# Kernel optimization log

Hardware: AMD Instinct MI355X
Metric: run time of the kernel (lower is better)

Reference implementation:

```python
import jax, jax.numpy as jnp
import numpy as np

B, S, N, H, E = 512, 96, 64, 512, 512  # batch, seq_len, nodes(c_in), hidden, edges/graph


def setup_inputs() -> dict:
    key = jax.random.key(0)
    ks = jax.random.split(key, 6)
    x = jax.random.normal(ks[0], (B, S, N), jnp.float32)
    edge_index = jax.random.randint(ks[1], (B, 2, E), 0, N, dtype=jnp.int32)
    W1 = jax.random.normal(ks[2], (H, S), jnp.float32) * 0.05   # gcn1 lin weight [out,in]
    b1 = jnp.zeros((H,), jnp.float32)
    W2 = jax.random.normal(ks[3], (S, H), jnp.float32) * 0.05   # gcn2 lin weight
    b2 = jnp.zeros((S,), jnp.float32)
    conv_w = jax.random.normal(ks[4], (H, N, 3), jnp.float32) * 0.05  # Conv1d [out,in,k]
    return {"x": x, "edge_index": edge_index, "W1": W1, "b1": b1,
            "W2": W2, "b2": b2, "conv_w": conv_w}


def _gcn(h, src, dst, W, b, n):
    # PyG GCNConv: h' = D^-1/2 (A+I) D^-1/2 (h W^T) + b  (self-loops already in src/dst)
    h = h @ W.T                                       # [n, out]
    ones = jnp.ones(src.shape[0], h.dtype)
    deg = jax.ops.segment_sum(ones, dst, num_segments=n)
    dinv = jnp.where(deg > 0, jax.lax.rsqrt(deg), 0.0)
    norm = dinv[src] * dinv[dst]                      # [e]
    out = jax.ops.segment_sum(h[src] * norm[:, None], dst, num_segments=n)
    return out + b


def reference(x, edge_index, W1, b1, W2, b2, conv_w):
    b, s, n = x.shape
    loops = jnp.broadcast_to(jnp.arange(n, dtype=edge_index.dtype), (b, n))
    src = jnp.concatenate([edge_index[:, 0, :], loops], axis=1)  # add self-loops
    dst = jnp.concatenate([edge_index[:, 1, :], loops], axis=1)

    def per_graph(xb, sb, db):
        h = _gcn(xb.T, sb, db, W1, b1, n)   # [n, H]
        h = jax.nn.relu(h)
        h = _gcn(h, sb, db, W2, b2, n)      # [n, s]
        return h                             # channels-first [c_in, L]

    h = jax.vmap(per_graph)(x, src, dst)    # [b, n, s]
    # TokenEmbedding: Conv1d kernel=3, circular padding=1, no bias
    hp = jnp.pad(h, ((0, 0), (0, 0), (1, 1)), mode='wrap')
    y = jax.lax.conv_general_dilated(hp, conv_w, (1,), 'VALID',
                                     dimension_numbers=('NCH', 'OIH', 'NCH'))  # [b, H, s]
    return jnp.transpose(y, (0, 2, 1))      # [b, s, H]; dropout = identity (eval)
```

## Files before the change

### kernel.cpp

```cpp
#include <hip/hip_runtime.h>
#include <hip/hip_bf16.h>

#define BB 512
#define SS 96
#define NN 64
#define HH 512
#define EE 512

typedef __attribute__((ext_vector_type(8))) short short8;
typedef __attribute__((ext_vector_type(4))) float f32x4;

__device__ __forceinline__ unsigned short f2bf(float f) {
    union { float f; unsigned u; } v; v.f = f;
    return (unsigned short)((v.u + 0x7FFFu + ((v.u >> 16) & 1u)) >> 16);
}
__device__ __forceinline__ ushort4 f4bf(float4 v) {
    ushort4 u; u.x = f2bf(v.x); u.y = f2bf(v.y); u.z = f2bf(v.z); u.w = f2bf(v.w);
    return u;
}

__global__ __launch_bounds__(256) void k_mega(const float* __restrict__ x,
                                              const int* __restrict__ ei,
                                              const float* __restrict__ W1,
                                              const float* __restrict__ b1,
                                              const float* __restrict__ W2,
                                              const float* __restrict__ b2,
                                              unsigned short* __restrict__ H2T) {
    const int b = blockIdx.x, t = threadIdx.x;
    const int wave = t >> 6, lane = t & 63, quad = lane >> 4, l16 = lane & 15;

    __shared__ __align__(16) char smem[59392];
    unsigned short* As   = (unsigned short*)smem;
    unsigned short* XsW2 = (unsigned short*)(smem + 9216);
    unsigned short* Gs   = (unsigned short*)(smem + 23040);
    unsigned short* W1sT = (unsigned short*)(smem + 36352);
    float*          Asm  = (float*)(smem + 36352);
    unsigned short* H1s  = (unsigned short*)(smem + 49664);
    int*            deg  = (int*)(smem + 58880);
    float*          dinv = (float*)(smem + 59136);

    for (int i = t; i < 4096; i += 256) Asm[i] = 0.f;
    if (t < NN) deg[t] = 1;
    __syncthreads();
    const int* eb = ei + (size_t)b * 2 * EE;
    for (int e = t; e < EE; e += 256) atomicAdd(&deg[eb[EE + e]], 1);
    __syncthreads();
    if (t < NN) dinv[t] = rsqrtf((float)deg[t]);
    __syncthreads();
    for (int e = t; e < EE; e += 256) {
        int s = eb[e], d = eb[EE + e];
        atomicAdd(&Asm[d * 64 + s], dinv[s] * dinv[d]);
    }
    if (t < NN) atomicAdd(&Asm[t * 64 + t], dinv[t] * dinv[t]);
    __syncthreads();

    for (int i = t; i < 1024; i += 256) {
        int n = i >> 4, m4 = (i & 15) * 4;
        *(ushort4*)(As + n * 72 + m4) = f4bf(*(const float4*)(Asm + n * 64 + m4));
    }
    const float* xb = x + (size_t)b * SS * NN;
    for (int i = t; i < 96 * 16; i += 256) {
        int s = i >> 4, c4 = (i & 15) * 4;
        *(ushort4*)(XsW2 + s * 72 + c4) = f4bf(*(const float4*)(xb + s * 64 + c4));
    }
    __syncthreads();

    {
        short8 a0 = *(const short8*)(As + (wave * 16 + l16) * 72 + quad * 8);
        short8 a1 = *(const short8*)(As + (wave * 16 + l16) * 72 + 32 + quad * 8);
        f32x4 acc0[6];
        #pragma unroll
        for (int j = 0; j < 6; ++j) acc0[j] = (f32x4){0.f, 0.f, 0.f, 0.f};
        #pragma unroll
        for (int j = 0; j < 6; ++j) {
            short8 bb0 = *(const short8*)(XsW2 + (j * 16 + l16) * 72 + quad * 8);
            short8 bb1 = *(const short8*)(XsW2 + (j * 16 + l16) * 72 + 32 + quad * 8);
            acc0[j] = __builtin_amdgcn_mfma_f32_16x16x32_bf16(a0, bb0, acc0[j], 0, 0, 0);
            acc0[j] = __builtin_amdgcn_mfma_f32_16x16x32_bf16(a1, bb1, acc0[j], 0, 0, 0);
        }
        #pragma unroll
        for (int j = 0; j < 6; ++j)
            #pragma unroll
            for (int r = 0; r < 4; ++r)
                Gs[(wave * 16 + quad * 4 + r) * 104 + j * 16 + l16] = f2bf(acc0[j][r]);
    }

    f32x4 accT[6];
    #pragma unroll
    for (int j = 0; j < 6; ++j) accT[j] = (f32x4){0.f, 0.f, 0.f, 0.f};

    for (int hc = 0; hc < 8; ++hc) {
        __syncthreads();
        for (int i = t; i < 64 * 24; i += 256) {
            int row = i / 24, c4 = (i % 24) * 4;
            *(ushort4*)(W1sT + row * 104 + c4) =
                f4bf(*(const float4*)(W1 + (size_t)(hc * 64 + row) * 96 + c4));
        }
        for (int i = t; i < 96 * 16; i += 256) {
            int row = i >> 4, c4 = (i & 15) * 4;
            *(ushort4*)(XsW2 + row * 72 + c4) =
                f4bf(*(const float4*)(W2 + (size_t)row * HH + hc * 64 + c4));
        }
        __syncthreads();
        short8 ga[3];
        #pragma unroll
        for (int kc = 0; kc < 3; ++kc)
            ga[kc] = *(const short8*)(Gs + (wave * 16 + l16) * 104 + kc * 32 + quad * 8);
        f32x4 acc1[4];
        #pragma unroll
        for (int j = 0; j < 4; ++j) acc1[j] = (f32x4){0.f, 0.f, 0.f, 0.f};
        #pragma unroll
        for (int j = 0; j < 4; ++j)
            #pragma unroll
            for (int kc = 0; kc < 3; ++kc) {
                short8 bb = *(const short8*)(W1sT + (j * 16 + l16) * 104 + kc * 32 + quad * 8);
                acc1[j] = __builtin_amdgcn_mfma_f32_16x16x32_bf16(ga[kc], bb, acc1[j], 0, 0, 0);
            }
        float bias[4];
        #pragma unroll
        for (int j = 0; j < 4; ++j) bias[j] = b1[hc * 64 + j * 16 + l16];
        #pragma unroll
        for (int j = 0; j < 4; ++j)
            #pragma unroll
            for (int r = 0; r < 4; ++r)
                H1s[(wave * 16 + quad * 4 + r) * 72 + j * 16 + l16] =
                    f2bf(fmaxf(acc1[j][r] + bias[j], 0.f));
        __syncthreads();
        short8 ha0 = *(const short8*)(H1s + (wave * 16 + l16) * 72 + quad * 8);
        short8 ha1 = *(const short8*)(H1s + (wave * 16 + l16) * 72 + 32 + quad * 8);
        #pragma unroll
        for (int j = 0; j < 6; ++j) {
            short8 bb0 = *(const short8*)(XsW2 + (j * 16 + l16) * 72 + quad * 8);
            short8 bb1 = *(const short8*)(XsW2 + (j * 16 + l16) * 72 + 32 + quad * 8);
            accT[j] = __builtin_amdgcn_mfma_f32_16x16x32_bf16(ha0, bb0, accT[j], 0, 0, 0);
            accT[j] = __builtin_amdgcn_mfma_f32_16x16x32_bf16(ha1, bb1, accT[j], 0, 0, 0);
        }
    }
    __syncthreads();

    #pragma unroll
    for (int j = 0; j < 6; ++j)
        #pragma unroll
        for (int r = 0; r < 4; ++r)
            W1sT[(j * 16 + l16) * 72 + wave * 16 + quad * 4 + r] = f2bf(accT[j][r]);
    __syncthreads();

    {
        short8 a0 = *(const short8*)(As + (wave * 16 + l16) * 72 + quad * 8);
        short8 a1 = *(const short8*)(As + (wave * 16 + l16) * 72 + 32 + quad * 8);
        f32x4 acc3[6];
        #pragma unroll
        for (int j = 0; j < 6; ++j) acc3[j] = (f32x4){0.f, 0.f, 0.f, 0.f};
        #pragma unroll
        for (int j = 0; j < 6; ++j) {
            short8 t0 = *(const short8*)(W1sT + (j * 16 + l16) * 72 + quad * 8);
            short8 t1 = *(const short8*)(W1sT + (j * 16 + l16) * 72 + 32 + quad * 8);
            acc3[j] = __builtin_amdgcn_mfma_f32_16x16x32_bf16(a0, t0, acc3[j], 0, 0, 0);
            acc3[j] = __builtin_amdgcn_mfma_f32_16x16x32_bf16(a1, t1, acc3[j], 0, 0, 0);
        }
        unsigned short* Hb = H2T + (size_t)b * SS * NN;
        #pragma unroll
        for (int j = 0; j < 6; ++j) {
            float bb2 = b2[j * 16 + l16];
            #pragma unroll
            for (int r = 0; r < 4; ++r)
                Hb[(j * 16 + l16) * NN + wave * 16 + quad * 4 + r] = f2bf(acc3[j][r] + bb2);
        }
    }
}

__global__ __launch_bounds__(256) void k_conv(const unsigned short* __restrict__ H2T,
                                              const float* __restrict__ cw,
                                              float* __restrict__ out) {
    const int hb = blockIdx.x, b = blockIdx.y, t = threadIdx.x;
    const int wave = t >> 6, lane = t & 63, quad = lane >> 4, l16 = lane & 15;
    const int h0 = hb * 64;

    __shared__ __align__(16) unsigned short Wc[64 * 200];
    __shared__ __align__(16) unsigned short Hp[98 * 72];

    for (int i = t; i < 64 * 48; i += 256) {
        int row = i / 48, c4 = (i % 48) * 4;
        float4 v = *(const float4*)(cw + (size_t)(h0 + row) * 192 + c4);
        float vv[4] = {v.x, v.y, v.z, v.w};
        #pragma unroll
        for (int q = 0; q < 4; ++q) {
            int kap = c4 + q, n = kap / 3, kw = kap % 3;
            Wc[row * 200 + kw * 64 + n] = f2bf(vv[q]);
        }
    }
    const unsigned short* Hsrc = H2T + (size_t)b * SS * NN;
    for (int i = t; i < 98 * 8; i += 256) {
        int sp = i >> 3, c8 = (i & 7) * 8;
        int s = (sp == 0) ? 95 : ((sp == 97) ? 0 : sp - 1);
        *(short8*)(Hp + sp * 72 + c8) = *(const short8*)(Hsrc + s * NN + c8);
    }
    __syncthreads();

    short8 a[6];
    #pragma unroll
    for (int kc = 0; kc < 6; ++kc)
        a[kc] = *(const short8*)(Wc + (wave * 16 + l16) * 200 + kc * 32 + quad * 8);

    f32x4 acc[6];
    #pragma unroll
    for (int j = 0; j < 6; ++j) acc[j] = (f32x4){0.f, 0.f, 0.f, 0.f};

    #pragma unroll
    for (int j = 0; j < 6; ++j) {
        #pragma unroll
        for (int kc = 0; kc < 6; ++kc) {
            int kw = kc >> 1, nb = (kc & 1) * 32;
            int sp = j * 16 + l16 + kw;
            short8 bf = *(const short8*)(Hp + sp * 72 + nb + quad * 8);
            acc[j] = __builtin_amdgcn_mfma_f32_16x16x32_bf16(a[kc], bf, acc[j], 0, 0, 0);
        }
    }

    float* ob = out + (size_t)b * SS * HH;
    #pragma unroll
    for (int j = 0; j < 6; ++j)
        #pragma unroll
        for (int r = 0; r < 4; ++r)
            ob[(size_t)(j * 16 + l16) * HH + h0 + wave * 16 + quad * 4 + r] = acc[j][r];
}

extern "C" void kernel_launch(void* const* d_in, const int* in_sizes, int n_in,
                              void* d_out, int out_size, void* d_ws, size_t ws_size,
                              hipStream_t stream) {
    const float* x  = (const float*)d_in[0];
    const int*   ei = (const int*)d_in[1];
    const float* W1 = (const float*)d_in[2];
    const float* b1 = (const float*)d_in[3];
    const float* W2 = (const float*)d_in[4];
    const float* b2 = (const float*)d_in[5];
    const float* cw = (const float*)d_in[6];
    float* out = (float*)d_out;

    unsigned short* H2T = (unsigned short*)d_ws;

    k_mega<<<BB, 256, 0, stream>>>(x, ei, W1, b1, W2, b2, H2T);
    dim3 gc(8, BB);
    k_conv<<<gc, 256, 0, stream>>>(H2T, cw, out);
}
```

Before: 212.5 us.

## Split fused GCN megakernel into batched GEMM stages with pre-converted bf16 weights

Replaces the per-graph megakernel with a pipeline: a prep kernel converts W1, W2 and the conv weights to bf16 once, then separate kernels build A and G=A·X, run H1=relu(G·W1ᵀ) as a large batched GEMM over all nodes, run T=W2·H1ᵀ, apply A again, and do the conv. The goal is to stop every block from re-reading and re-converting the full weight matrices, and to get better MFMA tiling on the big GEMMs. In exchange it adds kernel launches and round-trips intermediates (H1, T) through global memory, using the output buffer as scratch for H1. The conv kernel now reads operands straight from global memory instead of staging them in LDS, and writes its output with float4 stores.

```diff
diff --git a/kernel.cpp b/kernel.cpp
--- a/kernel.cpp
+++ b/kernel.cpp
@@ -9,220 +9,237 @@
 
 typedef __attribute__((ext_vector_type(8))) short short8;
 typedef __attribute__((ext_vector_type(4))) float f32x4;
-
-__device__ __forceinline__ unsigned short f2bf(float f) {
+typedef unsigned short u16;
+
+__device__ __forceinline__ u16 f2bf(float f) {
     union { float f; unsigned u; } v; v.f = f;
-    return (unsigned short)((v.u + 0x7FFFu + ((v.u >> 16) & 1u)) >> 16);
-}
-__device__ __forceinline__ ushort4 f4bf(float4 v) {
-    ushort4 u; u.x = f2bf(v.x); u.y = f2bf(v.y); u.z = f2bf(v.z); u.w = f2bf(v.w);
-    return u;
-}
-
-__global__ __launch_bounds__(256) void k_mega(const float* __restrict__ x,
-                                              const int* __restrict__ ei,
-                                              const float* __restrict__ W1,
-                                              const float* __restrict__ b1,
+    return (u16)((v.u + 0x7FFFu + ((v.u >> 16) & 1u)) >> 16);
+}
+__device__ __forceinline__ short8 ld8bf(const u16* p) { return *(const short8*)p; }
+__device__ __forceinline__ short8 cvt8(const float* p) {
+    float4 a = *(const float4*)p, b = *(const float4*)(p + 4);
+    short8 r;
+    r[0] = (short)f2bf(a.x); r[1] = (short)f2bf(a.y);
+    r[2] = (short)f2bf(a.z); r[3] = (short)f2bf(a.w);
+    r[4] = (short)f2bf(b.x); r[5] = (short)f2bf(b.y);
+    r[6] = (short)f2bf(b.z); r[7] = (short)f2bf(b.w);
+    return r;
+}
+
+__global__ __launch_bounds__(256) void k_prep(const float* __restrict__ W1,
                                               const float* __restrict__ W2,
-                                              const float* __restrict__ b2,
-                                              unsigned short* __restrict__ H2T) {
+                                              const float* __restrict__ cw,
+                                              u16* __restrict__ W1b,
+                                              u16* __restrict__ W2b,
+                                              u16* __restrict__ Wcb) {
+    const int i0 = blockIdx.x * 256 + threadIdx.x, stp = gridDim.x * 256;
+    for (int i = i0; i < HH * SS; i += stp) W1b[i] = f2bf(W1[i]);
+    for (int i = i0; i < SS * HH; i += stp) W2b[i] = f2bf(W2[i]);
+    for (int i = i0; i < HH * 192; i += stp) {
+        int h = i / 192, q = i % 192, n = q / 3, kw = q % 3;
+        Wcb[h * 192 + kw * 64 + n] = f2bf(cw[i]);
+    }
+}
+
+__global__ __launch_bounds__(256) void k_AG(const float* __restrict__ x,
+                                            const int* __restrict__ ei,
+                                            u16* __restrict__ Ab,
+                                            u16* __restrict__ G) {
     const int b = blockIdx.x, t = threadIdx.x;
     const int wave = t >> 6, lane = t & 63, quad = lane >> 4, l16 = lane & 15;
-
-    __shared__ __align__(16) char smem[59392];
-    unsigned short* As   = (unsigned short*)smem;
-    unsigned short* XsW2 = (unsigned short*)(smem + 9216);
-    unsigned short* Gs   = (unsigned short*)(smem + 23040);
-    unsigned short* W1sT = (unsigned short*)(smem + 36352);
-    float*          Asm  = (float*)(smem + 36352);
-    unsigned short* H1s  = (unsigned short*)(smem + 49664);
-    int*            deg  = (int*)(smem + 58880);
-    float*          dinv = (float*)(smem + 59136);
+    __shared__ float Asm[4096];
+    __shared__ int   deg[64];
+    __shared__ float dinv[64];
 
     for (int i = t; i < 4096; i += 256) Asm[i] = 0.f;
-    if (t < NN) deg[t] = 1;
+    if (t < 64) deg[t] = 1;
     __syncthreads();
     const int* eb = ei + (size_t)b * 2 * EE;
     for (int e = t; e < EE; e += 256) atomicAdd(&deg[eb[EE + e]], 1);
     __syncthreads();
-    if (t < NN) dinv[t] = rsqrtf((float)deg[t]);
+    if (t < 64) dinv[t] = rsqrtf((float)deg[t]);
     __syncthreads();
     for (int e = t; e < EE; e += 256) {
         int s = eb[e], d = eb[EE + e];
         atomicAdd(&Asm[d * 64 + s], dinv[s] * dinv[d]);
     }
-    if (t < NN) atomicAdd(&Asm[t * 64 + t], dinv[t] * dinv[t]);
-    __syncthreads();
-
-    for (int i = t; i < 1024; i += 256) {
-        int n = i >> 4, m4 = (i & 15) * 4;
-        *(ushort4*)(As + n * 72 + m4) = f4bf(*(const float4*)(Asm + n * 64 + m4));
-    }
+    if (t < 64) atomicAdd(&Asm[t * 64 + t], dinv[t] * dinv[t]);
+    __syncthreads();
+
+    u16* Abb = Ab + (size_t)b * 4096;
+    for (int i = t; i < 4096; i += 256) Abb[i] = f2bf(Asm[i]);
+
+    short8 af[2];
+    af[0] = cvt8(&Asm[(wave * 16 + l16) * 64 + quad * 8]);
+    af[1] = cvt8(&Asm[(wave * 16 + l16) * 64 + 32 + quad * 8]);
+
     const float* xb = x + (size_t)b * SS * NN;
-    for (int i = t; i < 96 * 16; i += 256) {
-        int s = i >> 4, c4 = (i & 15) * 4;
-        *(ushort4*)(XsW2 + s * 72 + c4) = f4bf(*(const float4*)(xb + s * 64 + c4));
-    }
-    __syncthreads();
-
-    {
-        short8 a0 = *(const short8*)(As + (wave * 16 + l16) * 72 + quad * 8);
-        short8 a1 = *(const short8*)(As + (wave * 16 + l16) * 72 + 32 + quad * 8);
-        f32x4 acc0[6];
-        #pragma unroll
-        for (int j = 0; j < 6; ++j) acc0[j] = (f32x4){0.f, 0.f, 0.f, 0.f};
-        #pragma unroll
-        for (int j = 0; j < 6; ++j) {
-            short8 bb0 = *(const short8*)(XsW2 + (j * 16 + l16) * 72 + quad * 8);
-            short8 bb1 = *(const short8*)(XsW2 + (j * 16 + l16) * 72 + 32 + quad * 8);
-            acc0[j] = __builtin_amdgcn_mfma_f32_16x16x32_bf16(a0, bb0, acc0[j], 0, 0, 0);
-            acc0[j] = __builtin_amdgcn_mfma_f32_16x16x32_bf16(a1, bb1, acc0[j], 0, 0, 0);
-        }
-        #pragma unroll
-        for (int j = 0; j < 6; ++j)
+    f32x4 acc[6];
+    #pragma unroll
+    for (int j = 0; j < 6; ++j) acc[j] = (f32x4){0.f, 0.f, 0.f, 0.f};
+    #pragma unroll
+    for (int j = 0; j < 6; ++j)
+        #pragma unroll
+        for (int kc = 0; kc < 2; ++kc) {
+            short8 bb = cvt8(xb + (j * 16 + l16) * 64 + kc * 32 + quad * 8);
+            acc[j] = __builtin_amdgcn_mfma_f32_16x16x32_bf16(af[kc], bb, acc[j], 0, 0, 0);
+        }
+    u16* Gb = G + (size_t)b * NN * SS;
+    #pragma unroll
+    for (int j = 0; j < 6; ++j)
+        #pragma unroll
+        for (int r = 0; r < 4; ++r)
+            Gb[(wave * 16 + quad * 4 + r) * 96 + j * 16 + l16] = f2bf(acc[j][r]);
+}
+
+__global__ __launch_bounds__(256) void k_h1(const u16* __restrict__ G,
+                                            const u16* __restrict__ W1b,
+                                            const float* __restrict__ b1,
+                                            u16* __restrict__ H1) {
+    const int t = threadIdx.x;
+    const int h0 = blockIdx.x * 128, m0 = blockIdx.y * 128;
+    const int wave = t >> 6, lane = t & 63, quad = lane >> 4, l16 = lane & 15;
+    const int wm = wave >> 1, wn = wave & 1;
+
+    f32x4 acc[4][4];
+    #pragma unroll
+    for (int i = 0; i < 4; ++i)
+        #pragma unroll
+        for (int j = 0; j < 4; ++j) acc[i][j] = (f32x4){0.f, 0.f, 0.f, 0.f};
+
+    #pragma unroll
+    for (int kc = 0; kc < 3; ++kc) {
+        short8 a[4], bf[4];
+        #pragma unroll
+        for (int i = 0; i < 4; ++i)
+            a[i] = ld8bf(G + (size_t)(m0 + wm * 64 + i * 16 + l16) * 96 + kc * 32 + quad * 8);
+        #pragma unroll
+        for (int j = 0; j < 4; ++j)
+            bf[j] = ld8bf(W1b + (size_t)(h0 + wn * 64 + j * 16 + l16) * 96 + kc * 32 + quad * 8);
+        #pragma unroll
+        for (int i = 0; i < 4; ++i)
+            #pragma unroll
+            for (int j = 0; j < 4; ++j)
+                acc[i][j] = __builtin_amdgcn_mfma_f32_16x16x32_bf16(a[i], bf[j], acc[i][j], 0, 0, 0);
+    }
+
+    float bj[4];
+    #pragma unroll
+    for (int j = 0; j < 4; ++j) bj[j] = b1[h0 + wn * 64 + j * 16 + l16];
+
+    #pragma unroll
+    for (int i = 0; i < 4; ++i)
+        #pragma unroll
+        for (int j = 0; j < 4; ++j) {
+            int h = h0 + wn * 64 + j * 16 + l16;
+            #pragma unroll
+            for (int r = 0; r < 4; ++r) {
+                int m = m0 + wm * 64 + i * 16 + quad * 4 + r;
+                H1[(size_t)m * HH + h] = f2bf(fmaxf(acc[i][j][r] + bj[j], 0.f));
+            }
+        }
+}
+
+__global__ __launch_bounds__(256) void k_tT(const u16* __restrict__ H1,
+                                            const u16* __restrict__ W2b,
+                                            u16* __restrict__ Tt) {
+    const int t = threadIdx.x, m0 = blockIdx.x * 64;
+    const int wave = t >> 6, lane = t & 63, quad = lane >> 4, l16 = lane & 15;
+    const int wm = wave >> 1, wn = wave & 1;
+
+    f32x4 acc[3][2];
+    #pragma unroll
+    for (int i = 0; i < 3; ++i)
+        #pragma unroll
+        for (int j = 0; j < 2; ++j) acc[i][j] = (f32x4){0.f, 0.f, 0.f, 0.f};
+
+    for (int kc = 0; kc < 16; ++kc) {
+        short8 a[3], bf[2];
+        #pragma unroll
+        for (int i = 0; i < 3; ++i)
+            a[i] = ld8bf(W2b + (size_t)(wm * 48 + i * 16 + l16) * HH + kc * 32 + quad * 8);
+        #pragma unroll
+        for (int j = 0; j < 2; ++j)
+            bf[j] = ld8bf(H1 + (size_t)(m0 + wn * 32 + j * 16 + l16) * HH + kc * 32 + quad * 8);
+        #pragma unroll
+        for (int i = 0; i < 3; ++i)
+            #pragma unroll
+            for (int j = 0; j < 2; ++j)
+                acc[i][j] = __builtin_amdgcn_mfma_f32_16x16x32_bf16(a[i], bf[j], acc[i][j], 0, 0, 0);
+    }
+
+    #pragma unroll
+    for (int i = 0; i < 3; ++i)
+        #pragma unroll
+        for (int j = 0; j < 2; ++j)
             #pragma unroll
             for (int r = 0; r < 4; ++r)
-                Gs[(wave * 16 + quad * 4 + r) * 104 + j * 16 + l16] = f2bf(acc0[j][r]);
-    }
-
-    f32x4 accT[6];
-    #pragma unroll
-    for (int j = 0; j < 6; ++j) accT[j] = (f32x4){0.f, 0.f, 0.f, 0.f};
-
-    for (int hc = 0; hc < 8; ++hc) {
-        __syncthreads();
-        for (int i = t; i < 64 * 24; i += 256) {
-            int row = i / 24, c4 = (i % 24) * 4;
-            *(ushort4*)(W1sT + row * 104 + c4) =
-                f4bf(*(const float4*)(W1 + (size_t)(hc * 64 + row) * 96 + c4));
-        }
-        for (int i = t; i < 96 * 16; i += 256) {
-            int row = i >> 4, c4 = (i & 15) * 4;
-            *(ushort4*)(XsW2 + row * 72 + c4) =
-                f4bf(*(const float4*)(W2 + (size_t)row * HH + hc * 64 + c4));
-        }
-        __syncthreads();
-        short8 ga[3];
-        #pragma unroll
-        for (int kc = 0; kc < 3; ++kc)
-            ga[kc] = *(const short8*)(Gs + (wave * 16 + l16) * 104 + kc * 32 + quad * 8);
-        f32x4 acc1[4];
-        #pragma unroll
-        for (int j = 0; j < 4; ++j) acc1[j] = (f32x4){0.f, 0.f, 0.f, 0.f};
-        #pragma unroll
-        for (int j = 0; j < 4; ++j)
-            #pragma unroll
-            for (int kc = 0; kc < 3; ++kc) {
-                short8 bb = *(const short8*)(W1sT + (j * 16 + l16) * 104 + kc * 32 + quad * 8);
-                acc1[j] = __builtin_amdgcn_mfma_f32_16x16x32_bf16(ga[kc], bb, acc1[j], 0, 0, 0);
-            }
-        float bias[4];
-        #pragma unroll
-        for (int j = 0; j < 4; ++j) bias[j] = b1[hc * 64 + j * 16 + l16];
-        #pragma unroll
-        for (int j = 0; j < 4; ++j)
-            #pragma unroll
-            for (int r = 0; r < 4; ++r)
-                H1s[(wave * 16 + quad * 4 + r) * 72 + j * 16 + l16] =
-                    f2bf(fmaxf(acc1[j][r] + bias[j], 0.f));
-        __syncthreads();
-        short8 ha0 = *(const short8*)(H1s + (wave * 16 + l16) * 72 + quad * 8);
-        short8 ha1 = *(const short8*)(H1s + (wave * 16 + l16) * 72 + 32 + quad * 8);
-        #pragma unroll
-        for (int j = 0; j < 6; ++j) {
-            short8 bb0 = *(const short8*)(XsW2 + (j * 16 + l16) * 72 + quad * 8);
-            short8 bb1 = *(const short8*)(XsW2 + (j * 16 + l16) * 72 + 32 + quad * 8);
-            accT[j] = __builtin_amdgcn_mfma_f32_16x16x32_bf16(ha0, bb0, accT[j], 0, 0, 0);
-            accT[j] = __builtin_amdgcn_mfma_f32_16x16x32_bf16(ha1, bb1, accT[j], 0, 0, 0);
-        }
-    }
-    __syncthreads();
-
-    #pragma unroll
-    for (int j = 0; j < 6; ++j)
-        #pragma unroll
-        for (int r = 0; r < 4; ++r)
-            W1sT[(j * 16 + l16) * 72 + wave * 16 + quad * 4 + r] = f2bf(accT[j][r]);
-    __syncthreads();
-
-    {
-        short8 a0 = *(const short8*)(As + (wave * 16 + l16) * 72 + quad * 8);
-        short8 a1 = *(const short8*)(As + (wave * 16 + l16) * 72 + 32 + quad * 8);
-        f32x4 acc3[6];
-        #pragma unroll
-        for (int j = 0; j < 6; ++j) acc3[j] = (f32x4){0.f, 0.f, 0.f, 0.f};
-        #pragma unroll
-        for (int j = 0; j < 6; ++j) {
-            short8 t0 = *(const short8*)(W1sT + (j * 16 + l16) * 72 + quad * 8);
-            short8 t1 = *(const short8*)(W1sT + (j * 16 + l16) * 72 + 32 + quad * 8);
-            acc3[j] = __builtin_amdgcn_mfma_f32_16x16x32_bf16(a0, t0, acc3[j], 0, 0, 0);
-            acc3[j] = __builtin_amdgcn_mfma_f32_16x16x32_bf16(a1, t1, acc3[j], 0, 0, 0);
-        }
-        unsigned short* Hb = H2T + (size_t)b * SS * NN;
-        #pragma unroll
-        for (int j = 0; j < 6; ++j) {
-            float bb2 = b2[j * 16 + l16];
-            #pragma unroll
-            for (int r = 0; r < 4; ++r)
-                Hb[(j * 16 + l16) * NN + wave * 16 + quad * 4 + r] = f2bf(acc3[j][r] + bb2);
-        }
-    }
-}
-
-__global__ __launch_bounds__(256) void k_conv(const unsigned short* __restrict__ H2T,
-                                              const float* __restrict__ cw,
+                Tt[(size_t)(wm * 48 + i * 16 + quad * 4 + r) * 32768
+                   + m0 + wn * 32 + j * 16 + l16] = f2bf(acc[i][j][r]);
+}
+
+__global__ __launch_bounds__(256) void k_h2(const u16* __restrict__ Tt,
+                                            const u16* __restrict__ Ab,
+                                            const float* __restrict__ b2,
+                                            u16* __restrict__ H2T) {
+    const int b = blockIdx.x, t = threadIdx.x;
+    const int wave = t >> 6, lane = t & 63, quad = lane >> 4, l16 = lane & 15;
+
+    short8 bf[2];
+    #pragma unroll
+    for (int kc = 0; kc < 2; ++kc)
+        bf[kc] = ld8bf(Ab + (size_t)b * 4096 + (wave * 16 + l16) * 64 + kc * 32 + quad * 8);
+
+    f32x4 acc[6];
+    #pragma unroll
+    for (int i = 0; i < 6; ++i) acc[i] = (f32x4){0.f, 0.f, 0.f, 0.f};
+    #pragma unroll
+    for (int i = 0; i < 6; ++i)
+        #pragma unroll
+        for (int kc = 0; kc < 2; ++kc) {
+            short8 aa = ld8bf(Tt + (size_t)(i * 16 + l16) * 32768 + b * 64 + kc * 32 + quad * 8);
+            acc[i] = __builtin_amdgcn_mfma_f32_16x16x32_bf16(aa, bf[kc], acc[i], 0, 0, 0);
+        }
+
+    u16* Hb = H2T + (size_t)b * SS * NN;
+    #pragma unroll
+    for (int i = 0; i < 6; ++i)
+        #pragma unroll
+        for (int r = 0; r < 4; ++r) {
+            int s = i * 16 + quad * 4 + r;
+            Hb[s * 64 + wave * 16 + l16] = f2bf(acc[i][r] + b2[s]);
+        }
+}
+
+__global__ __launch_bounds__(256) void k_conv(const u16* __restrict__ H2T,
+                                              const u16* __restrict__ Wcb,
                                               float* __restrict__ out) {
     const int hb = blockIdx.x, b = blockIdx.y, t = threadIdx.x;
     const int wave = t >> 6, lane = t & 63, quad = lane >> 4, l16 = lane & 15;
     const int h0 = hb * 64;
 
-    __shared__ __align__(16) unsigned short Wc[64 * 200];
-    __shared__ __align__(16) unsigned short Hp[98 * 72];
-
-    for (int i = t; i < 64 * 48; i += 256) {
-        int row = i / 48, c4 = (i % 48) * 4;
-        float4 v = *(const float4*)(cw + (size_t)(h0 + row) * 192 + c4);
-        float vv[4] = {v.x, v.y, v.z, v.w};
-        #pragma unroll
-        for (int q = 0; q < 4; ++q) {
-            int kap = c4 + q, n = kap / 3, kw = kap % 3;
-            Wc[row * 200 + kw * 64 + n] = f2bf(vv[q]);
-        }
-    }
-    const unsigned short* Hsrc = H2T + (size_t)b * SS * NN;
-    for (int i = t; i < 98 * 8; i += 256) {
-        int sp = i >> 3, c8 = (i & 7) * 8;
-        int s = (sp == 0) ? 95 : ((sp == 97) ? 0 : sp - 1);
-        *(short8*)(Hp + sp * 72 + c8) = *(const short8*)(Hsrc + s * NN + c8);
-    }
-    __syncthreads();
-
     short8 a[6];
     #pragma unroll
     for (int kc = 0; kc < 6; ++kc)
-        a[kc] = *(const short8*)(Wc + (wave * 16 + l16) * 200 + kc * 32 + quad * 8);
-
-    f32x4 acc[6];
-    #pragma unroll
-    for (int j = 0; j < 6; ++j) acc[j] = (f32x4){0.f, 0.f, 0.f, 0.f};
+        a[kc] = ld8bf(Wcb + (size_t)(h0 + wave * 16 + l16) * 192 + kc * 32 + quad * 8);
+
+    const u16* Hg = H2T + (size_t)b * SS * NN;
+    float* ob = out + (size_t)b * SS * HH;
 
     #pragma unroll
     for (int j = 0; j < 6; ++j) {
+        f32x4 acc = (f32x4){0.f, 0.f, 0.f, 0.f};
         #pragma unroll
         for (int kc = 0; kc < 6; ++kc) {
             int kw = kc >> 1, nb = (kc & 1) * 32;
-            int sp = j * 16 + l16 + kw;
-            short8 bf = *(const short8*)(Hp + sp * 72 + nb + quad * 8);
-            acc[j] = __builtin_amdgcn_mfma_f32_16x16x32_bf16(a[kc], bf, acc[j], 0, 0, 0);
-        }
-    }
-
-    float* ob = out + (size_t)b * SS * HH;
-    #pragma unroll
-    for (int j = 0; j < 6; ++j)
-        #pragma unroll
-        for (int r = 0; r < 4; ++r)
-            ob[(size_t)(j * 16 + l16) * HH + h0 + wave * 16 + quad * 4 + r] = acc[j][r];
+            int s2 = j * 16 + l16 + kw - 1;
+            s2 = (s2 < 0) ? 95 : ((s2 > 95) ? 0 : s2);
+            short8 bf = ld8bf(Hg + s2 * 64 + nb + quad * 8);
+            acc = __builtin_amdgcn_mfma_f32_16x16x32_bf16(a[kc], bf, acc, 0, 0, 0);
+        }
+        float4 vv = {acc[0], acc[1], acc[2], acc[3]};
+        *(float4*)(ob + (size_t)(j * 16 + l16) * HH + h0 + wave * 16 + quad * 4) = vv;
+    }
 }
 
 extern "C" void kernel_launch(void* const* d_in, const int* in_sizes, int n_in,
@@ -237,9 +254,22 @@
     const float* cw = (const float*)d_in[6];
     float* out = (float*)d_out;
 
-    unsigned short* H2T = (unsigned short*)d_ws;
-
-    k_mega<<<BB, 256, 0, stream>>>(x, ei, W1, b1, W2, b2, H2T);
+    char* w = (char*)d_ws;
+    u16* Ab  = (u16*)w;
+    u16* G   = (u16*)(w + 4194304);
+    u16* Tt  = G;
+    u16* H2T = (u16*)(w + 10485760);
+    u16* W1b = (u16*)(w + 16777216);
+    u16* W2b = (u16*)(w + 16875520);
+    u16* Wcb = (u16*)(w + 16973824);
+    u16* H1  = (u16*)d_out;
+
+    k_prep<<<192, 256, 0, stream>>>(W1, W2, cw, W1b, W2b, Wcb);
+    k_AG  <<<BB, 256, 0, stream>>>(x, ei, Ab, G);
+    dim3 g1(4, 256);
+    k_h1  <<<g1, 256, 0, stream>>>(G, W1b, b1, H1);
+    k_tT  <<<BB, 256, 0, stream>>>(H1, W2b, Tt);
+    k_h2  <<<BB, 256, 0, stream>>>(Tt, Ab, b2, H2T);
     dim3 gc(8, BB);
-    k_conv<<<gc, 256, 0, stream>>>(H2T, cw, out);
-}
+    k_conv<<<gc, 256, 0, stream>>>(H2T, Wcb, out);
+}
```

Result: slower. 245.7 us (+15.6%).
